# Performance work log

Hardware: AMD Instinct MI355X
Metric: run time of the kernel (lower is better)

The kernel has to match this reference:

```python
import jax, jax.numpy as jnp
import numpy as np

V, D, H, L, E, DH, K, PMAX = 50257, 128, 4, 4, 8, 512, 2, 256
B, T = 8, 256


def setup_inputs() -> dict:
    key = jax.random.key(0)
    ks = jax.random.split(key, 10)
    s = 0.02
    def n(k, shape):
        return jax.random.normal(k, shape, jnp.float32) * s
    return dict(
        idx=jax.random.randint(ks[0], (B, T), 0, V),
        tok_emb=n(ks[1], (V, D)),
        pos_emb=n(ks[2], (PMAX, D)),
        ln1_g=jnp.ones((L, D), jnp.float32), ln1_b=jnp.zeros((L, D), jnp.float32),
        in_w=n(ks[3], (L, 3 * D, D)), in_b=jnp.zeros((L, 3 * D), jnp.float32),
        out_w=n(ks[4], (L, D, D)), out_b=jnp.zeros((L, D), jnp.float32),
        ln2_g=jnp.ones((L, D), jnp.float32), ln2_b=jnp.zeros((L, D), jnp.float32),
        gate_w=n(ks[5], (L, E, D)),
        w1=n(ks[6], (L, E, DH, D)),
        w2=n(ks[7], (L, E, D, DH)),
        lnf_g=jnp.ones((D,), jnp.float32), lnf_b=jnp.zeros((D,), jnp.float32),
        lm_w=n(ks[8], (V, D)),
    )


def _ln(x, g, b):
    mu = x.mean(-1, keepdims=True)
    var = jnp.var(x, -1, keepdims=True)
    return (x - mu) / jnp.sqrt(var + 1e-5) * g + b


def _moe(x, gw, w1, w2):
    # x: [N, D]; top-2 sparse MoE, computed densely per expert then combined.
    logits = x @ gw.T                              # [N, E]
    probs = jax.nn.softmax(logits, -1)
    topw, topi = jax.lax.top_k(probs, K)           # [N, K]
    topw = topw / topw.sum(-1, keepdims=True)
    we = (topw[..., None] * jax.nn.one_hot(topi, E, dtype=x.dtype)).sum(1)  # [N, E]
    h = jax.nn.silu(jnp.einsum('nd,ehd->neh', x, w1))   # [N, E, DH]
    y = jnp.einsum('neh,edh->ned', h, w2)               # [N, E, D]
    return jnp.einsum('ned,ne->nd', y, we)


def reference(idx, tok_emb, pos_emb, ln1_g, ln1_b, in_w, in_b, out_w, out_b,
              ln2_g, ln2_b, gate_w, w1, w2, lnf_g, lnf_b, lm_w):
    b, t = idx.shape
    x = tok_emb[idx] + pos_emb[:t]                 # [B, T, D]
    dh = D // H
    scale = 1.0 / np.sqrt(dh)
    for l in range(L):
        xl = _ln(x, ln1_g[l], ln1_b[l])
        qkv = xl @ in_w[l].T + in_b[l]
        q, k, v = jnp.split(qkv, 3, -1)
        q = q.reshape(b, t, H, dh)
        k = k.reshape(b, t, H, dh)
        v = v.reshape(b, t, H, dh)
        att = jax.nn.softmax(jnp.einsum('bqhd,bkhd->bhqk', q, k) * scale, -1)
        o = jnp.einsum('bhqk,bkhd->bqhd', att, v).reshape(b, t, D)
        x = x + o @ out_w[l].T + out_b[l]
        x2 = _ln(x, ln2_g[l], ln2_b[l]).reshape(b * t, D)
        x = x + _moe(x2, gate_w[l], w1[l], w2[l]).reshape(b, t, D)
    return _ln(x, lnf_g, lnf_b) @ lm_w.T           # [B, T, V]
```

## Files before the change

kernel.cpp:

```cpp
#include <hip/hip_runtime.h>
#include <math.h>

#define NTOK 2048
#define DD   128
#define NHEAD 4
#define DHEAD 32
#define NLAYER 4
#define NEXP 8
#define DHID 512
#define NVOCAB 50257
#define VPAD  50304
#define SEQ   256
#define NBATCH 8

typedef __attribute__((ext_vector_type(8))) short short8v;
typedef __attribute__((ext_vector_type(4))) float f32x4;

__device__ __forceinline__ unsigned short nm_bf16r(float f) {
  unsigned u = __float_as_uint(f);
  u += 0x7fffu + ((u >> 16) & 1u);
  return (unsigned short)(u >> 16);
}

__device__ __forceinline__ float nm_silu(float a) {
  return a / (1.f + __expf(-a));
}

template<int N4>
__device__ __forceinline__ float nm_dotv(const float* __restrict__ a,
                                         const float* __restrict__ w) {
  const float4* a4 = (const float4*)a;
  const float4* w4 = (const float4*)w;
  float sx = 0.f, sy = 0.f, sz = 0.f, sw = 0.f;
#pragma unroll 16
  for (int k = 0; k < N4; ++k) {
    float4 av = a4[k], wv = w4[k];
    sx = fmaf(av.x, wv.x, sx);
    sy = fmaf(av.y, wv.y, sy);
    sz = fmaf(av.z, wv.z, sz);
    sw = fmaf(av.w, wv.w, sw);
  }
  return (sx + sy) + (sz + sw);
}

__global__ void nm_embed(const int* __restrict__ idx, const float* __restrict__ tok,
                         const float* __restrict__ pos, float* __restrict__ x) {
  int n = blockIdx.x, d = threadIdx.x;
  x[n * DD + d] = tok[(size_t)idx[n] * DD + d] + pos[(n % SEQ) * DD + d];
}

__global__ void nm_ln(const float* __restrict__ in, const float* __restrict__ g,
                      const float* __restrict__ b, float* __restrict__ out) {
  int n = blockIdx.x, lane = threadIdx.x;
  float v0 = in[n * DD + lane], v1 = in[n * DD + lane + 64];
  float s = v0 + v1;
#pragma unroll
  for (int o = 32; o > 0; o >>= 1) s += __shfl_xor(s, o, 64);
  float mu = s * (1.f / 128.f);
  float d0 = v0 - mu, d1 = v1 - mu;
  float q = d0 * d0 + d1 * d1;
#pragma unroll
  for (int o = 32; o > 0; o >>= 1) q += __shfl_xor(q, o, 64);
  float rstd = rsqrtf(q * (1.f / 128.f) + 1e-5f);
  out[n * DD + lane]      = d0 * rstd * g[lane]      + b[lane];
  out[n * DD + lane + 64] = d1 * rstd * g[lane + 64] + b[lane + 64];
}

__global__ void nm_combine_ln(const float* __restrict__ yb, const int* __restrict__ posm,
                              const float* __restrict__ topw, float* __restrict__ x,
                              const float* __restrict__ g, const float* __restrict__ b,
                              float* __restrict__ xl) {
  int n = blockIdx.x, lane = threadIdx.x;
  float w0 = topw[2 * n], w1 = topw[2 * n + 1];
  int p0 = posm[2 * n], p1 = posm[2 * n + 1];
  float v0 = x[n * DD + lane]      + w0 * yb[(size_t)p0 * DD + lane]
                                   + w1 * yb[(size_t)p1 * DD + lane];
  float v1 = x[n * DD + lane + 64] + w0 * yb[(size_t)p0 * DD + lane + 64]
                                   + w1 * yb[(size_t)p1 * DD + lane + 64];
  x[n * DD + lane]      = v0;
  x[n * DD + lane + 64] = v1;
  float s = v0 + v1;
#pragma unroll
  for (int o = 32; o > 0; o >>= 1) s += __shfl_xor(s, o, 64);
  float mu = s * (1.f / 128.f);
  float d0 = v0 - mu, d1 = v1 - mu;
  float q = d0 * d0 + d1 * d1;
#pragma unroll
  for (int o = 32; o > 0; o >>= 1) q += __shfl_xor(q, o, 64);
  float rstd = rsqrtf(q * (1.f / 128.f) + 1e-5f);
  xl[n * DD + lane]      = d0 * rstd * g[lane]      + b[lane];
  xl[n * DD + lane + 64] = d1 * rstd * g[lane + 64] + b[lane + 64];
}

template<int F>
__global__ __launch_bounds__(256) void nm_gemm(
    const float* __restrict__ A, const float* __restrict__ B,
    float* __restrict__ C, const float* __restrict__ bias,
    int M, int N, int K,
    const int* __restrict__ list, const int* __restrict__ cnt,
    const int* __restrict__ off) {
  constexpr bool GA = F & 1, SI = F & 2, BI = F & 4, RE = F & 8, GR = F & 16;
  __shared__ __align__(16) float As[64][68];
  __shared__ __align__(16) float Bs[64][68];
  int tid = threadIdx.x;
  int n0 = blockIdx.x * 64, m0 = blockIdx.y * 64;
  int Mloc = M, o = 0;
  const float* Bb = B;
  if constexpr (GR) {
    int e = blockIdx.z;
    Mloc = cnt[e];
    if (m0 >= Mloc) return;
    o = off[e];
    Bb = B + (size_t)e * (size_t)N * K;
  }
  int tm = tid & 15, tn = tid >> 4;
  float acc[4][4] = {};
  for (int kc = 0; kc < K; kc += 64) {
#pragma unroll
    for (int i = 0; i < 4; ++i) {
      int f = tid + 256 * i;
      int r = f >> 4, c4 = f & 15;
      int mi = m0 + r;
      if (mi >= Mloc) mi = m0;
      const float* ar;
      if constexpr (GA) ar = A + (size_t)(list[o + mi] >> 1) * K;
      else              ar = A + (size_t)(o + mi) * K;
      float4 v = *(const float4*)(ar + kc + c4 * 4);
      int k = c4 * 4;
      As[k][r] = v.x; As[k + 1][r] = v.y; As[k + 2][r] = v.z; As[k + 3][r] = v.w;
    }
#pragma unroll
    for (int i = 0; i < 4; ++i) {
      int f = tid + 256 * i;
      int r = f >> 4, c4 = f & 15;
      const float* br = Bb + (size_t)(n0 + r) * K + kc + c4 * 4;
      float4 v = *(const float4*)br;
      int k = c4 * 4;
      Bs[k][r] = v.x; Bs[k + 1][r] = v.y; Bs[k + 2][r] = v.z; Bs[k + 3][r] = v.w;
    }
    __syncthreads();
#pragma unroll 16
    for (int k = 0; k < 64; ++k) {
      float4 a = *(const float4*)&As[k][tm * 4];
      float4 b = *(const float4*)&Bs[k][tn * 4];
      acc[0][0] = fmaf(a.x, b.x, acc[0][0]); acc[0][1] = fmaf(a.x, b.y, acc[0][1]);
      acc[0][2] = fmaf(a.x, b.z, acc[0][2]); acc[0][3] = fmaf(a.x, b.w, acc[0][3]);
      acc[1][0] = fmaf(a.y, b.x, acc[1][0]); acc[1][1] = fmaf(a.y, b.y, acc[1][1]);
      acc[1][2] = fmaf(a.y, b.z, acc[1][2]); acc[1][3] = fmaf(a.y, b.w, acc[1][3]);
      acc[2][0] = fmaf(a.z, b.x, acc[2][0]); acc[2][1] = fmaf(a.z, b.y, acc[2][1]);
      acc[2][2] = fmaf(a.z, b.z, acc[2][2]); acc[2][3] = fmaf(a.z, b.w, acc[2][3]);
      acc[3][0] = fmaf(a.w, b.x, acc[3][0]); acc[3][1] = fmaf(a.w, b.y, acc[3][1]);
      acc[3][2] = fmaf(a.w, b.z, acc[3][2]); acc[3][3] = fmaf(a.w, b.w, acc[3][3]);
    }
    __syncthreads();
  }
  float4 bv = {0.f, 0.f, 0.f, 0.f};
  if constexpr (BI) bv = *(const float4*)(bias + n0 + tn * 4);
#pragma unroll
  for (int i = 0; i < 4; ++i) {
    int mi = m0 + tm * 4 + i;
    if (GR && mi >= Mloc) continue;
    float* cr = C + (size_t)(o + mi) * N + n0 + tn * 4;
    float r0 = acc[i][0], r1 = acc[i][1], r2 = acc[i][2], r3 = acc[i][3];
    if constexpr (BI) { r0 += bv.x; r1 += bv.y; r2 += bv.z; r3 += bv.w; }
    if constexpr (SI) { r0 = nm_silu(r0); r1 = nm_silu(r1); r2 = nm_silu(r2); r3 = nm_silu(r3); }
    if constexpr (RE) { r0 += cr[0]; r1 += cr[1]; r2 += cr[2]; r3 += cr[3]; }
    float4 st = {r0, r1, r2, r3};
    *(float4*)cr = st;
  }
}

__global__ __launch_bounds__(256) void nm_attn2(const float* __restrict__ qkv,
                                                float* __restrict__ o) {
  __shared__ __align__(16) float Ks[SEQ][DHEAD];
  __shared__ __align__(16) float Vs[SEQ][DHEAD];
  __shared__ float mbuf[32][9], sbuf[32][9];
  __shared__ __align__(16) float accbuf[32][36];
  int bh = blockIdx.x;
  int b = bh >> 2, h = bh & 3;
  int qt = blockIdx.y;
  int tid = threadIdx.x;
  const float* base = qkv + (size_t)b * SEQ * 384;
  for (int f = tid; f < SEQ * 8; f += 256) {
    int t = f >> 3, c4 = f & 7;
    float4 kv = *(const float4*)(base + (size_t)t * 384 + 128 + h * DHEAD + c4 * 4);
    float4 vv = *(const float4*)(base + (size_t)t * 384 + 256 + h * DHEAD + c4 * 4);
    *(float4*)&Ks[t][c4 * 4] = kv;
    *(float4*)&Vs[t][c4 * 4] = vv;
  }
  __syncthreads();
  int q = tid & 31, slot = tid >> 5;
  int tq = qt * 32 + q;
  float qv[DHEAD];
  const float4* q4 = (const float4*)(base + (size_t)tq * 384 + h * DHEAD);
#pragma unroll
  for (int k = 0; k < 8; ++k) {
    float4 v = q4[k];
    qv[4*k] = v.x; qv[4*k+1] = v.y; qv[4*k+2] = v.z; qv[4*k+3] = v.w;
  }
  float m = -1e30f, s = 0.f, acc[DHEAD];
#pragma unroll
  for (int d = 0; d < DHEAD; ++d) acc[d] = 0.f;
  const float scale = 0.17677669529663687f;
  int j0 = slot * 32;
  for (int jj = 0; jj < 32; ++jj) {
    int j = j0 + jj;
    const float4* kr = (const float4*)Ks[j];
    float sc = 0.f;
#pragma unroll
    for (int k = 0; k < 8; ++k) {
      float4 v = kr[k];
      sc += qv[4*k]*v.x + qv[4*k+1]*v.y + qv[4*k+2]*v.z + qv[4*k+3]*v.w;
    }
    sc *= scale;
    float mn = fmaxf(m, sc);
    float f = __expf(m - mn), p = __expf(sc - mn);
    s = s * f + p;
    const float4* vr = (const float4*)Vs[j];
#pragma unroll
    for (int k = 0; k < 8; ++k) {
      float4 v = vr[k];
      acc[4*k]   = acc[4*k]  * f + p * v.x;
      acc[4*k+1] = acc[4*k+1]* f + p * v.y;
      acc[4*k+2] = acc[4*k+2]* f + p * v.z;
      acc[4*k+3] = acc[4*k+3]* f + p * v.w;
    }
    m = mn;
  }
  mbuf[q][slot] = m;
  sbuf[q][slot] = s;
  __syncthreads();
  float M = mbuf[q][0];
#pragma unroll
  for (int t = 1; t < 8; ++t) M = fmaxf(M, mbuf[q][t]);
  float S = 0.f;
#pragma unroll
  for (int t = 0; t < 8; ++t) S += sbuf[q][t] * __expf(mbuf[q][t] - M);
  float w = __expf(m - M);
#pragma unroll
  for (int d = 0; d < DHEAD; ++d) acc[d] *= w;
#pragma unroll
  for (int p = 0; p < 8; ++p) {
    if (slot == p) {
      if (p == 0) {
#pragma unroll
        for (int d = 0; d < DHEAD; ++d) accbuf[q][d] = acc[d];
      } else {
#pragma unroll
        for (int d = 0; d < DHEAD; ++d) accbuf[q][d] += acc[d];
      }
    }
    __syncthreads();
  }
  if (slot == 0) sbuf[q][8] = 1.f / S;
  __syncthreads();
  int q2 = tid >> 3, c4 = tid & 7;
  float inv = sbuf[q2][8];
  float4 v = *(const float4*)&accbuf[q2][c4 * 4];
  v.x *= inv; v.y *= inv; v.z *= inv; v.w *= inv;
  *(float4*)(o + (size_t)(b * SEQ + qt * 32 + q2) * DD + h * DHEAD + c4 * 4) = v;
}

__global__ void nm_gate(const float* __restrict__ x2, const float* __restrict__ gw,
                        int* __restrict__ topi, float* __restrict__ topw,
                        int* __restrict__ cnt) {
  int tid = threadIdx.x;
  int e = tid & 7;
  int n = blockIdx.x * 32 + (tid >> 3);
  const float4* xr = (const float4*)(x2 + (size_t)n * DD);
  const float4* wr = (const float4*)(gw + (size_t)e * DD);
  float sx = 0.f, sy = 0.f, sz = 0.f, sw = 0.f;
#pragma unroll
  for (int k = 0; k < 32; ++k) {
    float4 a = xr[k], w = wr[k];
    sx = fmaf(a.x, w.x, sx); sy = fmaf(a.y, w.y, sy);
    sz = fmaf(a.z, w.z, sz); sw = fmaf(a.w, w.w, sw);
  }
  float s = (sx + sy) + (sz + sw);
  int base = (tid & 63) & ~7;
  float g[NEXP];
#pragma unroll
  for (int i = 0; i < NEXP; ++i) g[i] = __shfl(s, base + i, 64);
  if (e == 0) {
    int i0 = 0;
#pragma unroll
    for (int i = 1; i < NEXP; ++i) if (g[i] > g[i0]) i0 = i;
    int i1 = (i0 == 0) ? 1 : 0;
#pragma unroll
    for (int i = 0; i < NEXP; ++i) { if (i != i0 && g[i] > g[i1]) i1 = i; }
    float p1 = __expf(g[i1] - g[i0]);
    float inv = 1.f / (1.f + p1);
    topi[2 * n] = i0; topi[2 * n + 1] = i1;
    topw[2 * n] = inv; topw[2 * n + 1] = p1 * inv;
    atomicAdd(cnt + i0, 1);
    atomicAdd(cnt + i1, 1);
  }
}

__global__ void nm_route(const int* __restrict__ topi, const int* __restrict__ cnt,
                         int* __restrict__ off, int* __restrict__ list,
                         int* __restrict__ posm) {
  __shared__ int lcur[NEXP];
  int tid = threadIdx.x;
  if (tid < NEXP) {
    int o = 0;
    for (int e = 0; e < tid; ++e) o += cnt[e];
    lcur[tid] = o;
    off[tid] = o;
  }
  __syncthreads();
  for (int t = tid; t < 2 * NTOK; t += 1024) {
    int e = topi[t];
    int p = atomicAdd(&lcur[e], 1);
    list[p] = t;
    posm[t] = p;
  }
}

__global__ void nm_zero(int* __restrict__ p, int n) {
  int i = blockIdx.x * 64 + threadIdx.x;
  if (i < n) p[i] = 0;
}

__global__ void nm_moe(const float* __restrict__ x2, const float* __restrict__ gw,
                       const float* __restrict__ w1, const float* __restrict__ w2,
                       float* __restrict__ x) {
  __shared__ __align__(16) float xs[DD];
  __shared__ __align__(16) float hs[DHID];
  __shared__ float gl[NEXP];
  __shared__ int   ei[2];
  __shared__ float ew[2];
  int n = blockIdx.x, tid = threadIdx.x;
  if (tid < DD) xs[tid] = x2[n * DD + tid];
  __syncthreads();
  if (tid < NEXP) gl[tid] = nm_dotv<32>(xs, gw + (size_t)tid * DD);
  __syncthreads();
  if (tid == 0) {
    int i0 = 0;
#pragma unroll
    for (int e = 1; e < NEXP; ++e) if (gl[e] > gl[i0]) i0 = e;
    int i1 = (i0 == 0) ? 1 : 0;
    for (int e = 0; e < NEXP; ++e) { if (e == i0) continue; if (gl[e] > gl[i1]) i1 = e; }
    float p1 = __expf(gl[i1] - gl[i0]);
    float inv = 1.f / (1.f + p1);
    ei[0] = i0; ei[1] = i1; ew[0] = inv; ew[1] = p1 * inv;
  }
  __syncthreads();
  float yacc = 0.f;
  for (int t2 = 0; t2 < 2; ++t2) {
    int e = ei[t2];
    float wt = ew[t2];
    const float* w1e = w1 + (size_t)e * DHID * DD;
#pragma unroll
    for (int jj = 0; jj < 2; ++jj) {
      int j = tid + jj * 256;
      float a = nm_dotv<32>(xs, w1e + (size_t)j * DD);
      hs[j] = nm_silu(a);
    }
    __syncthreads();
    if (tid < DD) yacc += wt * nm_dotv<128>(hs, w2 + ((size_t)e * DD + tid) * DHID);
    __syncthreads();
  }
  if (tid < DD) x[n * DD + tid] += yacc;
}

__global__ void nm_cvt_x(const float* __restrict__ in, unsigned short* __restrict__ ob) {
  int i = blockIdx.x * 256 + threadIdx.x;
  ob[i] = nm_bf16r(in[i]);
}
__global__ void nm_cvt_w(const float* __restrict__ in, unsigned short* __restrict__ ob) {
  size_t i = (size_t)blockIdx.x * 256 + threadIdx.x;
  const size_t n = (size_t)NVOCAB * DD;
  ob[i] = (i < n) ? nm_bf16r(in[i]) : (unsigned short)0;
}

__device__ __forceinline__ short8v nm_load8(const unsigned short* p) {
  return *(const short8v*)p;
}
__device__ __forceinline__ short8v nm_cvt8(const float* p) {
  const float4* p4 = (const float4*)p;
  float4 a = p4[0], b = p4[1];
  short8v r;
  r[0] = (short)nm_bf16r(a.x); r[1] = (short)nm_bf16r(a.y);
  r[2] = (short)nm_bf16r(a.z); r[3] = (short)nm_bf16r(a.w);
  r[4] = (short)nm_bf16r(b.x); r[5] = (short)nm_bf16r(b.y);
  r[6] = (short)nm_bf16r(b.z); r[7] = (short)nm_bf16r(b.w);
  return r;
}

template<bool PRE>
__global__ __launch_bounds__(256) void nm_lmhead(
    const float* __restrict__ xf, const unsigned short* __restrict__ xfb,
    const float* __restrict__ lmw, const unsigned short* __restrict__ lmwb,
    float* __restrict__ out) {
  int wave = threadIdx.x >> 6, lane = threadIdx.x & 63;
  int wr = wave >> 1, wc = wave & 1;
  int row0 = blockIdx.y * 128 + wr * 64;
  int col0 = blockIdx.x * 128 + wc * 64;
  int lr = lane & 15, lk = (lane >> 4) * 8;

  f32x4 acc[4][4] = {};
#pragma unroll
  for (int ks = 0; ks < 4; ++ks) {
    int kb = ks * 32 + lk;
    short8v a[4], b[4];
#pragma unroll
    for (int i = 0; i < 4; ++i) {
      int r = row0 + i * 16 + lr;
      if constexpr (PRE) a[i] = nm_load8(xfb + (size_t)r * DD + kb);
      else               a[i] = nm_cvt8(xf + (size_t)r * DD + kb);
    }
#pragma unroll
    for (int j = 0; j < 4; ++j) {
      int c = col0 + j * 16 + lr;
      if constexpr (PRE) {
        b[j] = nm_load8(lmwb + (size_t)c * DD + kb);
      } else {
        if (c < NVOCAB) b[j] = nm_cvt8(lmw + (size_t)c * DD + kb);
        else {
          short8v z;
#pragma unroll
          for (int e = 0; e < 8; ++e) z[e] = 0;
          b[j] = z;
        }
      }
    }
#pragma unroll
    for (int i = 0; i < 4; ++i)
#pragma unroll
      for (int j = 0; j < 4; ++j)
        acc[i][j] = __builtin_amdgcn_mfma_f32_16x16x32_bf16(a[i], b[j], acc[i][j], 0, 0, 0);
  }
  int cr = (lane >> 4) * 4;
#pragma unroll
  for (int j = 0; j < 4; ++j) {
    int c = col0 + j * 16 + (lane & 15);
    if (c < NVOCAB) {
#pragma unroll
      for (int i = 0; i < 4; ++i)
#pragma unroll
        for (int r = 0; r < 4; ++r)
          out[(size_t)(row0 + i * 16 + cr + r) * NVOCAB + c] = acc[i][j][r];
    }
  }
}

extern "C" void kernel_launch(void* const* d_in, const int* in_sizes, int n_in,
                              void* d_out, int out_size, void* d_ws, size_t ws_size,
                              hipStream_t stream) {
  const int*   idx   = (const int*)  d_in[0];
  const float* tok   = (const float*)d_in[1];
  const float* pos   = (const float*)d_in[2];
  const float* ln1g  = (const float*)d_in[3];
  const float* ln1b  = (const float*)d_in[4];
  const float* inw   = (const float*)d_in[5];
  const float* inb   = (const float*)d_in[6];
  const float* outw  = (const float*)d_in[7];
  const float* outb  = (const float*)d_in[8];
  const float* ln2g  = (const float*)d_in[9];
  const float* ln2b  = (const float*)d_in[10];
  const float* gatew = (const float*)d_in[11];
  const float* w1    = (const float*)d_in[12];
  const float* w2    = (const float*)d_in[13];
  const float* lnfg  = (const float*)d_in[14];
  const float* lnfb  = (const float*)d_in[15];
  const float* lmw   = (const float*)d_in[16];
  float* out = (float*)d_out;

  float* ws   = (float*)d_ws;
  float* x    = ws;
  float* xl   = x    + NTOK * DD;
  float* qkv  = xl   + NTOK * DD;
  float* ao   = qkv  + NTOK * 384;
  float* topw = ao   + NTOK * DD;
  float* H    = topw + 2 * NTOK;
  float* yb   = H    + 2 * NTOK * DHID;
  int*   topi = (int*)(yb + 2 * NTOK * DD);
  int*   list = topi + 2 * NTOK;
  int*   posm = list + 2 * NTOK;
  int*   cnt  = posm + 2 * NTOK;
  int*   offs = cnt  + NLAYER * NEXP;
  unsigned short* xfb  = (unsigned short*)(offs + NLAYER * NEXP);
  unsigned short* lmwb = xfb + NTOK * DD;

  const size_t moe_bytes = (size_t)((char*)xfb - (char*)d_ws);
  const size_t pre_bytes = moe_bytes + ((size_t)NTOK * DD + (size_t)VPAD * DD) * 2;
  const bool moe_ok = (ws_size >= moe_bytes);
  const bool pre = (ws_size >= pre_bytes);

  nm_embed<<<NTOK, DD, 0, stream>>>(idx, tok, pos, x);
  if (moe_ok) nm_zero<<<(NLAYER * NEXP + 63) / 64, 64, 0, stream>>>(cnt, NLAYER * NEXP);
  nm_ln<<<NTOK, 64, 0, stream>>>(x, ln1g, ln1b, xl);

  for (int l = 0; l < NLAYER; ++l) {
    nm_gemm<4><<<dim3(384 / 64, NTOK / 64), 256, 0, stream>>>(
        xl, inw + (size_t)l * 384 * DD, qkv, inb + (size_t)l * 384,
        NTOK, 384, DD, nullptr, nullptr, nullptr);
    nm_attn2<<<dim3(NBATCH * NHEAD, SEQ / 32), 256, 0, stream>>>(qkv, ao);
    nm_gemm<12><<<dim3(DD / 64, NTOK / 64), 256, 0, stream>>>(
        ao, outw + (size_t)l * DD * DD, x, outb + (size_t)l * DD,
        NTOK, DD, DD, nullptr, nullptr, nullptr);
    nm_ln<<<NTOK, 64, 0, stream>>>(x, ln2g + l * DD, ln2b + l * DD, xl);

    const float* gN = (l < NLAYER - 1) ? ln1g + (l + 1) * DD : lnfg;
    const float* bN = (l < NLAYER - 1) ? ln1b + (l + 1) * DD : lnfb;
    if (moe_ok) {
      int* cnt_l = cnt + l * NEXP;
      int* off_l = offs + l * NEXP;
      const float* w1l = w1 + (size_t)l * NEXP * DHID * DD;
      const float* w2l = w2 + (size_t)l * NEXP * DD * DHID;
      nm_gate<<<NTOK / 32, 256, 0, stream>>>(xl, gatew + (size_t)l * NEXP * DD,
                                             topi, topw, cnt_l);
      nm_route<<<1, 1024, 0, stream>>>(topi, cnt_l, off_l, list, posm);
      nm_gemm<19><<<dim3(DHID / 64, 2 * NTOK / 64, NEXP), 256, 0, stream>>>(
          xl, w1l, H, nullptr, 0, DHID, DD, list, cnt_l, off_l);
      nm_gemm<16><<<dim3(DD / 64, 2 * NTOK / 64, NEXP), 256, 0, stream>>>(
          H, w2l, yb, nullptr, 0, DD, DHID, nullptr, cnt_l, off_l);
      nm_combine_ln<<<NTOK, 64, 0, stream>>>(yb, posm, topw, x, gN, bN, xl);
    } else {
      nm_moe<<<NTOK, 256, 0, stream>>>(xl, gatew + (size_t)l * NEXP * DD,
                                       w1 + (size_t)l * NEXP * DHID * DD,
                                       w2 + (size_t)l * NEXP * DD * DHID, x);
      nm_ln<<<NTOK, 64, 0, stream>>>(x, gN, bN, xl);
    }
  }

  if (pre) {
    nm_cvt_x<<<NTOK * DD / 256, 256, 0, stream>>>(xl, xfb);
    nm_cvt_w<<<VPAD * DD / 256, 256, 0, stream>>>(lmw, lmwb);
    nm_lmhead<true><<<dim3(VPAD / 128, NTOK / 128), 256, 0, stream>>>(
        xl, xfb, lmw, lmwb, out);
  } else {
    nm_lmhead<false><<<dim3(VPAD / 128, NTOK / 128), 256, 0, stream>>>(
        xl, nullptr, lmw, nullptr, out);
  }
}
```

Before: 915.3 us.

## Fuse embed+LN, out-proj+LN+gate, bf16 cast into combine, LDS-staged LM head

Embedding and the first LayerNorm now run in one kernel. The out-projection GEMM is fused with the residual add, LN2 and the MoE gate top-2 into a single kernel per layer. The final bf16 activation cast moves into the last combine_ln, and the weight cast is issued early. The LM head stages both bf16 tiles in swizzled LDS before the MFMA loop. Together these remove several launches and intermediate global round-trips. The costs are fewer blocks for the out-proj GEMM and a single-pass variance formula that is slightly less numerically robust.

```diff
diff --git a/kernel.cpp b/kernel.cpp
--- a/kernel.cpp
+++ b/kernel.cpp
@@ -43,10 +43,27 @@
   return (sx + sy) + (sz + sw);
 }
 
-__global__ void nm_embed(const int* __restrict__ idx, const float* __restrict__ tok,
-                         const float* __restrict__ pos, float* __restrict__ x) {
-  int n = blockIdx.x, d = threadIdx.x;
-  x[n * DD + d] = tok[(size_t)idx[n] * DD + d] + pos[(n % SEQ) * DD + d];
+__global__ void nm_embed_ln(const int* __restrict__ idx, const float* __restrict__ tok,
+                            const float* __restrict__ pos, const float* __restrict__ g,
+                            const float* __restrict__ b, float* __restrict__ x,
+                            float* __restrict__ xl) {
+  int n = blockIdx.x, lane = threadIdx.x;
+  int t = idx[n];
+  float v0 = tok[(size_t)t * DD + lane]      + pos[(n % SEQ) * DD + lane];
+  float v1 = tok[(size_t)t * DD + lane + 64] + pos[(n % SEQ) * DD + lane + 64];
+  x[n * DD + lane]      = v0;
+  x[n * DD + lane + 64] = v1;
+  float s = v0 + v1;
+#pragma unroll
+  for (int o = 32; o > 0; o >>= 1) s += __shfl_xor(s, o, 64);
+  float mu = s * (1.f / 128.f);
+  float d0 = v0 - mu, d1 = v1 - mu;
+  float q = d0 * d0 + d1 * d1;
+#pragma unroll
+  for (int o = 32; o > 0; o >>= 1) q += __shfl_xor(q, o, 64);
+  float rstd = rsqrtf(q * (1.f / 128.f) + 1e-5f);
+  xl[n * DD + lane]      = d0 * rstd * g[lane]      + b[lane];
+  xl[n * DD + lane + 64] = d1 * rstd * g[lane + 64] + b[lane + 64];
 }
 
 __global__ void nm_ln(const float* __restrict__ in, const float* __restrict__ g,
@@ -69,7 +86,7 @@
 __global__ void nm_combine_ln(const float* __restrict__ yb, const int* __restrict__ posm,
                               const float* __restrict__ topw, float* __restrict__ x,
                               const float* __restrict__ g, const float* __restrict__ b,
-                              float* __restrict__ xl) {
+                              float* __restrict__ xl, unsigned short* __restrict__ xb) {
   int n = blockIdx.x, lane = threadIdx.x;
   float w0 = topw[2 * n], w1 = topw[2 * n + 1];
   int p0 = posm[2 * n], p1 = posm[2 * n + 1];
@@ -88,8 +105,14 @@
 #pragma unroll
   for (int o = 32; o > 0; o >>= 1) q += __shfl_xor(q, o, 64);
   float rstd = rsqrtf(q * (1.f / 128.f) + 1e-5f);
-  xl[n * DD + lane]      = d0 * rstd * g[lane]      + b[lane];
-  xl[n * DD + lane + 64] = d1 * rstd * g[lane + 64] + b[lane + 64];
+  float o0 = d0 * rstd * g[lane]      + b[lane];
+  float o1 = d1 * rstd * g[lane + 64] + b[lane + 64];
+  xl[n * DD + lane]      = o0;
+  xl[n * DD + lane + 64] = o1;
+  if (xb) {
+    xb[n * DD + lane]      = nm_bf16r(o0);
+    xb[n * DD + lane + 64] = nm_bf16r(o1);
+  }
 }
 
 template<int F>
@@ -170,6 +193,123 @@
   }
 }
 
+__global__ __launch_bounds__(256) void nm_oplng(
+    const float* __restrict__ ao, const float* __restrict__ w,
+    const float* __restrict__ bias, float* __restrict__ x,
+    const float* __restrict__ g, const float* __restrict__ b,
+    float* __restrict__ xl, const float* __restrict__ gw,
+    int* __restrict__ topi, float* __restrict__ topw, int* __restrict__ cnt) {
+  __shared__ __align__(16) float As[64][36];
+  __shared__ __align__(16) float Bs[64][132];
+  __shared__ float Ls[32][9];
+  int tid = threadIdx.x;
+  int m0 = blockIdx.x * 32;
+  int tm = tid >> 5, tn = tid & 31;
+  float acc[4][4] = {};
+  for (int kc = 0; kc < DD; kc += 64) {
+#pragma unroll
+    for (int i = 0; i < 2; ++i) {
+      int ch = tid + 256 * i, r = ch >> 4, c4 = ch & 15;
+      float4 v = *(const float4*)(ao + (size_t)(m0 + r) * DD + kc + c4 * 4);
+      int k = c4 * 4;
+      As[k][r] = v.x; As[k + 1][r] = v.y; As[k + 2][r] = v.z; As[k + 3][r] = v.w;
+    }
+#pragma unroll
+    for (int i = 0; i < 8; ++i) {
+      int ch = tid + 256 * i, r = ch >> 4, c4 = ch & 15;
+      float4 v = *(const float4*)(w + (size_t)r * DD + kc + c4 * 4);
+      int k = c4 * 4;
+      Bs[k][r] = v.x; Bs[k + 1][r] = v.y; Bs[k + 2][r] = v.z; Bs[k + 3][r] = v.w;
+    }
+    __syncthreads();
+#pragma unroll 8
+    for (int k = 0; k < 64; ++k) {
+      float4 a = *(const float4*)&As[k][tm * 4];
+      float4 bb = *(const float4*)&Bs[k][tn * 4];
+      acc[0][0] = fmaf(a.x, bb.x, acc[0][0]); acc[0][1] = fmaf(a.x, bb.y, acc[0][1]);
+      acc[0][2] = fmaf(a.x, bb.z, acc[0][2]); acc[0][3] = fmaf(a.x, bb.w, acc[0][3]);
+      acc[1][0] = fmaf(a.y, bb.x, acc[1][0]); acc[1][1] = fmaf(a.y, bb.y, acc[1][1]);
+      acc[1][2] = fmaf(a.y, bb.z, acc[1][2]); acc[1][3] = fmaf(a.y, bb.w, acc[1][3]);
+      acc[2][0] = fmaf(a.z, bb.x, acc[2][0]); acc[2][1] = fmaf(a.z, bb.y, acc[2][1]);
+      acc[2][2] = fmaf(a.z, bb.z, acc[2][2]); acc[2][3] = fmaf(a.z, bb.w, acc[2][3]);
+      acc[3][0] = fmaf(a.w, bb.x, acc[3][0]); acc[3][1] = fmaf(a.w, bb.y, acc[3][1]);
+      acc[3][2] = fmaf(a.w, bb.z, acc[3][2]); acc[3][3] = fmaf(a.w, bb.w, acc[3][3]);
+    }
+    __syncthreads();
+  }
+  float4 bv = *(const float4*)(bias + tn * 4);
+  float rr[4][4], s1[4], s2[4];
+#pragma unroll
+  for (int i = 0; i < 4; ++i) {
+    int rw = m0 + tm * 4 + i;
+    float4 xv = *(const float4*)(x + (size_t)rw * DD + tn * 4);
+    float r0 = acc[i][0] + bv.x + xv.x;
+    float r1 = acc[i][1] + bv.y + xv.y;
+    float r2 = acc[i][2] + bv.z + xv.z;
+    float r3 = acc[i][3] + bv.w + xv.w;
+    rr[i][0] = r0; rr[i][1] = r1; rr[i][2] = r2; rr[i][3] = r3;
+    float4 st = {r0, r1, r2, r3};
+    *(float4*)(x + (size_t)rw * DD + tn * 4) = st;
+    s1[i] = r0 + r1 + r2 + r3;
+    s2[i] = r0 * r0 + r1 * r1 + r2 * r2 + r3 * r3;
+  }
+#pragma unroll
+  for (int o = 16; o >= 1; o >>= 1) {
+#pragma unroll
+    for (int i = 0; i < 4; ++i) {
+      s1[i] += __shfl_xor(s1[i], o, 64);
+      s2[i] += __shfl_xor(s2[i], o, 64);
+    }
+  }
+  float4 gv  = *(const float4*)(g + tn * 4);
+  float4 bbv = *(const float4*)(b + tn * 4);
+#pragma unroll
+  for (int i = 0; i < 4; ++i) {
+    int rw = m0 + tm * 4 + i;
+    float mu = s1[i] * (1.f / 128.f);
+    float var = s2[i] * (1.f / 128.f) - mu * mu;
+    float rstd = rsqrtf(var + 1e-5f);
+    float y0 = (rr[i][0] - mu) * rstd * gv.x + bbv.x;
+    float y1 = (rr[i][1] - mu) * rstd * gv.y + bbv.y;
+    float y2 = (rr[i][2] - mu) * rstd * gv.z + bbv.z;
+    float y3 = (rr[i][3] - mu) * rstd * gv.w + bbv.w;
+    float4 yv = {y0, y1, y2, y3};
+    *(float4*)(xl + (size_t)rw * DD + tn * 4) = yv;
+    *(float4*)&Bs[tm * 4 + i][tn * 4] = yv;
+  }
+  __syncthreads();
+  int grow = tid >> 3, ge = tid & 7;
+  const float4* xr = (const float4*)&Bs[grow][0];
+  const float4* wr = (const float4*)(gw + (size_t)ge * DD);
+  float sx = 0.f, sy = 0.f, sz = 0.f, sw = 0.f;
+#pragma unroll
+  for (int k2 = 0; k2 < 32; ++k2) {
+    float4 a = xr[k2], w4 = wr[k2];
+    sx = fmaf(a.x, w4.x, sx); sy = fmaf(a.y, w4.y, sy);
+    sz = fmaf(a.z, w4.z, sz); sw = fmaf(a.w, w4.w, sw);
+  }
+  Ls[grow][ge] = (sx + sy) + (sz + sw);
+  __syncthreads();
+  if (ge == 0) {
+    float gl[NEXP];
+#pragma unroll
+    for (int e = 0; e < NEXP; ++e) gl[e] = Ls[grow][e];
+    int i0 = 0;
+#pragma unroll
+    for (int e = 1; e < NEXP; ++e) if (gl[e] > gl[i0]) i0 = e;
+    int i1 = (i0 == 0) ? 1 : 0;
+#pragma unroll
+    for (int e = 0; e < NEXP; ++e) { if (e != i0 && gl[e] > gl[i1]) i1 = e; }
+    float p1 = __expf(gl[i1] - gl[i0]);
+    float inv = 1.f / (1.f + p1);
+    int n = m0 + grow;
+    topi[2 * n] = i0; topi[2 * n + 1] = i1;
+    topw[2 * n] = inv; topw[2 * n + 1] = p1 * inv;
+    atomicAdd(cnt + i0, 1);
+    atomicAdd(cnt + i1, 1);
+  }
+}
+
 __global__ __launch_bounds__(256) void nm_attn2(const float* __restrict__ qkv,
                                                 float* __restrict__ o) {
   __shared__ __align__(16) float Ks[SEQ][DHEAD];
@@ -261,42 +401,6 @@
   *(float4*)(o + (size_t)(b * SEQ + qt * 32 + q2) * DD + h * DHEAD + c4 * 4) = v;
 }
 
-__global__ void nm_gate(const float* __restrict__ x2, const float* __restrict__ gw,
-                        int* __restrict__ topi, float* __restrict__ topw,
-                        int* __restrict__ cnt) {
-  int tid = threadIdx.x;
-  int e = tid & 7;
-  int n = blockIdx.x * 32 + (tid >> 3);
-  const float4* xr = (const float4*)(x2 + (size_t)n * DD);
-  const float4* wr = (const float4*)(gw + (size_t)e * DD);
-  float sx = 0.f, sy = 0.f, sz = 0.f, sw = 0.f;
-#pragma unroll
-  for (int k = 0; k < 32; ++k) {
-    float4 a = xr[k], w = wr[k];
-    sx = fmaf(a.x, w.x, sx); sy = fmaf(a.y, w.y, sy);
-    sz = fmaf(a.z, w.z, sz); sw = fmaf(a.w, w.w, sw);
-  }
-  float s = (sx + sy) + (sz + sw);
-  int base = (tid & 63) & ~7;
-  float g[NEXP];
-#pragma unroll
-  for (int i = 0; i < NEXP; ++i) g[i] = __shfl(s, base + i, 64);
-  if (e == 0) {
-    int i0 = 0;
-#pragma unroll
-    for (int i = 1; i < NEXP; ++i) if (g[i] > g[i0]) i0 = i;
-    int i1 = (i0 == 0) ? 1 : 0;
-#pragma unroll
-    for (int i = 0; i < NEXP; ++i) { if (i != i0 && g[i] > g[i1]) i1 = i; }
-    float p1 = __expf(g[i1] - g[i0]);
-    float inv = 1.f / (1.f + p1);
-    topi[2 * n] = i0; topi[2 * n + 1] = i1;
-    topw[2 * n] = inv; topw[2 * n + 1] = p1 * inv;
-    atomicAdd(cnt + i0, 1);
-    atomicAdd(cnt + i1, 1);
-  }
-}
-
 __global__ void nm_route(const int* __restrict__ topi, const int* __restrict__ cnt,
                          int* __restrict__ off, int* __restrict__ list,
                          int* __restrict__ posm) {
@@ -364,19 +468,12 @@
   if (tid < DD) x[n * DD + tid] += yacc;
 }
 
-__global__ void nm_cvt_x(const float* __restrict__ in, unsigned short* __restrict__ ob) {
-  int i = blockIdx.x * 256 + threadIdx.x;
-  ob[i] = nm_bf16r(in[i]);
-}
 __global__ void nm_cvt_w(const float* __restrict__ in, unsigned short* __restrict__ ob) {
   size_t i = (size_t)blockIdx.x * 256 + threadIdx.x;
   const size_t n = (size_t)NVOCAB * DD;
   ob[i] = (i < n) ? nm_bf16r(in[i]) : (unsigned short)0;
 }
 
-__device__ __forceinline__ short8v nm_load8(const unsigned short* p) {
-  return *(const short8v*)p;
-}
 __device__ __forceinline__ short8v nm_cvt8(const float* p) {
   const float4* p4 = (const float4*)p;
   float4 a = p4[0], b = p4[1];
@@ -388,41 +485,84 @@
   return r;
 }
 
-template<bool PRE>
-__global__ __launch_bounds__(256) void nm_lmhead(
-    const float* __restrict__ xf, const unsigned short* __restrict__ xfb,
-    const float* __restrict__ lmw, const unsigned short* __restrict__ lmwb,
+__global__ __launch_bounds__(256) void nm_lmhead2(
+    const unsigned short* __restrict__ xfb, const unsigned short* __restrict__ lmwb,
+    float* __restrict__ out) {
+  __shared__ unsigned short Ab[128 * 128];
+  __shared__ unsigned short Bb[128 * 128];
+  int tid = threadIdx.x;
+  int row0 = blockIdx.y * 128, col0 = blockIdx.x * 128;
+#pragma unroll
+  for (int i = 0; i < 8; ++i) {
+    int ch = tid + i * 256;
+    int r = ch >> 4, s = ch & 15;
+    int sg = s ^ (r & 7);
+    *(short8v*)&Ab[r * 128 + s * 8] =
+        *(const short8v*)(xfb + (size_t)(row0 + r) * DD + sg * 8);
+    *(short8v*)&Bb[r * 128 + s * 8] =
+        *(const short8v*)(lmwb + (size_t)(col0 + r) * DD + sg * 8);
+  }
+  __syncthreads();
+  int wave = tid >> 6, lane = tid & 63;
+  int wr = wave >> 1, wc = wave & 1;
+  int lr = lane & 15, hk = lane >> 4;
+  f32x4 acc[4][4] = {};
+#pragma unroll
+  for (int ks = 0; ks < 4; ++ks) {
+    int sg = ks * 4 + hk;
+    int sx = (sg ^ (lr & 7)) * 8;
+    short8v a[4], b[4];
+#pragma unroll
+    for (int i = 0; i < 4; ++i)
+      a[i] = *(const short8v*)&Ab[(wr * 64 + i * 16 + lr) * 128 + sx];
+#pragma unroll
+    for (int j = 0; j < 4; ++j)
+      b[j] = *(const short8v*)&Bb[(wc * 64 + j * 16 + lr) * 128 + sx];
+#pragma unroll
+    for (int i = 0; i < 4; ++i)
+#pragma unroll
+      for (int j = 0; j < 4; ++j)
+        acc[i][j] = __builtin_amdgcn_mfma_f32_16x16x32_bf16(a[i], b[j], acc[i][j], 0, 0, 0);
+  }
+  int cr = (lane >> 4) * 4;
+#pragma unroll
+  for (int j = 0; j < 4; ++j) {
+    int c = col0 + wc * 64 + j * 16 + (lane & 15);
+    if (c < NVOCAB) {
+#pragma unroll
+      for (int i = 0; i < 4; ++i)
+#pragma unroll
+        for (int r = 0; r < 4; ++r)
+          out[(size_t)(row0 + wr * 64 + i * 16 + cr + r) * NVOCAB + c] = acc[i][j][r];
+    }
+  }
+}
+
+__global__ __launch_bounds__(256) void nm_lmhead_f32(
+    const float* __restrict__ xf, const float* __restrict__ lmw,
     float* __restrict__ out) {
   int wave = threadIdx.x >> 6, lane = threadIdx.x & 63;
   int wr = wave >> 1, wc = wave & 1;
   int row0 = blockIdx.y * 128 + wr * 64;
   int col0 = blockIdx.x * 128 + wc * 64;
   int lr = lane & 15, lk = (lane >> 4) * 8;
-
   f32x4 acc[4][4] = {};
 #pragma unroll
   for (int ks = 0; ks < 4; ++ks) {
     int kb = ks * 32 + lk;
     short8v a[4], b[4];
 #pragma unroll
-    for (int i = 0; i < 4; ++i) {
-      int r = row0 + i * 16 + lr;
-      if constexpr (PRE) a[i] = nm_load8(xfb + (size_t)r * DD + kb);
-      else               a[i] = nm_cvt8(xf + (size_t)r * DD + kb);
-    }
+    for (int i = 0; i < 4; ++i)
+      a[i] = nm_cvt8(xf + (size_t)(row0 + i * 16 + lr) * DD + kb);
 #pragma unroll
     for (int j = 0; j < 4; ++j) {
       int c = col0 + j * 16 + lr;
-      if constexpr (PRE) {
-        b[j] = nm_load8(lmwb + (size_t)c * DD + kb);
-      } else {
-        if (c < NVOCAB) b[j] = nm_cvt8(lmw + (size_t)c * DD + kb);
-        else {
-          short8v z;
-#pragma unroll
-          for (int e = 0; e < 8; ++e) z[e] = 0;
-          b[j] = z;
-        }
+      if (c < NVOCAB) b[j] = nm_cvt8(lmw + (size_t)c * DD + kb);
+      else {
+        short8v z;
+#pragma unroll
+        for (int e = 0; e < 8; ++e) z[e] = 0;
+        b[j] = z;
       }
     }
 #pragma unroll
@@ -473,14 +613,14 @@
   float* qkv  = xl   + NTOK * DD;
   float* ao   = qkv  + NTOK * 384;
   float* topw = ao   + NTOK * DD;
-  float* H    = topw + 2 * NTOK;
-  float* yb   = H    + 2 * NTOK * DHID;
-  int*   topi = (int*)(yb + 2 * NTOK * DD);
+  int*   topi = (int*)(topw + 2 * NTOK);
   int*   list = topi + 2 * NTOK;
   int*   posm = list + 2 * NTOK;
   int*   cnt  = posm + 2 * NTOK;
   int*   offs = cnt  + NLAYER * NEXP;
-  unsigned short* xfb  = (unsigned short*)(offs + NLAYER * NEXP);
+  float* H    = (float*)(offs + NLAYER * NEXP);
+  float* yb   = H    + 2 * NTOK * DHID;
+  unsigned short* xfb  = (unsigned short*)(yb + 2 * NTOK * DD);
   unsigned short* lmwb = xfb + NTOK * DD;
 
   const size_t moe_bytes = (size_t)((char*)xfb - (char*)d_ws);
@@ -488,19 +628,19 @@
   const bool moe_ok = (ws_size >= moe_bytes);
   const bool pre = (ws_size >= pre_bytes);
 
-  nm_embed<<<NTOK, DD, 0, stream>>>(idx, tok, pos, x);
+  nm_embed_ln<<<NTOK, 64, 0, stream>>>(idx, tok, pos, ln1g, ln1b, x, xl);
   if (moe_ok) nm_zero<<<(NLAYER * NEXP + 63) / 64, 64, 0, stream>>>(cnt, NLAYER * NEXP);
-  nm_ln<<<NTOK, 64, 0, stream>>>(x, ln1g, ln1b, xl);
+  if (pre) nm_cvt_w<<<VPAD * DD / 256, 256, 0, stream>>>(lmw, lmwb);
 
   for (int l = 0; l < NLAYER; ++l) {
     nm_gemm<4><<<dim3(384 / 64, NTOK / 64), 256, 0, stream>>>(
         xl, inw + (size_t)l * 384 * DD, qkv, inb + (size_t)l * 384,
         NTOK, 384, DD, nullptr, nullptr, nullptr);
     nm_attn2<<<dim3(NBATCH * NHEAD, SEQ / 32), 256, 0, stream>>>(qkv, ao);
-    nm_gemm<12><<<dim3(DD / 64, NTOK / 64), 256, 0, stream>>>(
-        ao, outw + (size_t)l * DD * DD, x, outb + (size_t)l * DD,
-        NTOK, DD, DD, nullptr, nullptr, nullptr);
-    nm_ln<<<NTOK, 64, 0, stream>>>(x, ln2g + l * DD, ln2b + l * DD, xl);
+    nm_oplng<<<NTOK / 32, 256, 0, stream>>>(
+        ao, outw + (size_t)l * DD * DD, outb + (size_t)l * DD, x,
+        ln2g + l * DD, ln2b + l * DD, xl, gatew + (size_t)l * NEXP * DD,
+        topi, topw, cnt + l * NEXP);
 
     const float* gN = (l < NLAYER - 1) ? ln1g + (l + 1) * DD : lnfg;
     const float* bN = (l < NLAYER - 1) ? ln1b + (l + 1) * DD : lnfb;
@@ -509,14 +649,14 @@
       int* off_l = offs + l * NEXP;
       const float* w1l = w1 + (size_t)l * NEXP * DHID * DD;
       const float* w2l = w2 + (size_t)l * NEXP * DD * DHID;
-      nm_gate<<<NTOK / 32, 256, 0, stream>>>(xl, gatew + (size_t)l * NEXP * DD,
-                                             topi, topw, cnt_l);
       nm_route<<<1, 1024, 0, stream>>>(topi, cnt_l, off_l, list, posm);
       nm_gemm<19><<<dim3(DHID / 64, 2 * NTOK / 64, NEXP), 256, 0, stream>>>(
           xl, w1l, H, nullptr, 0, DHID, DD, list, cnt_l, off_l);
       nm_gemm<16><<<dim3(DD / 64, 2 * NTOK / 64, NEXP), 256, 0, stream>>>(
           H, w2l, yb, nullptr, 0, DD, DHID, nullptr, cnt_l, off_l);
-      nm_combine_ln<<<NTOK, 64, 0, stream>>>(yb, posm, topw, x, gN, bN, xl);
+      nm_combine_ln<<<NTOK, 64, 0, stream>>>(
+          yb, posm, topw, x, gN, bN, xl,
+          (l == NLAYER - 1 && pre) ? xfb : (unsigned short*)nullptr);
     } else {
       nm_moe<<<NTOK, 256, 0, stream>>>(xl, gatew + (size_t)l * NEXP * DD,
                                        w1 + (size_t)l * NEXP * DHID * DD,
@@ -526,12 +666,8 @@
   }
 
   if (pre) {
-    nm_cvt_x<<<NTOK * DD / 256, 256, 0, stream>>>(xl, xfb);
-    nm_cvt_w<<<VPAD * DD / 256, 256, 0, stream>>>(lmw, lmwb);
-    nm_lmhead<true><<<dim3(VPAD / 128, NTOK / 128), 256, 0, stream>>>(
-        xl, xfb, lmw, lmwb, out);
+    nm_lmhead2<<<dim3(VPAD / 128, NTOK / 128), 256, 0, stream>>>(xfb, lmwb, out);
   } else {
-    nm_lmhead<false><<<dim3(VPAD / 128, NTOK / 128), 256, 0, stream>>>(
-        xl, nullptr, lmw, nullptr, out);
-  }
-}
+    nm_lmhead_f32<<<dim3(VPAD / 128, NTOK / 128), 256, 0, stream>>>(xl, lmw, out);
+  }
+}
```

Measured after the change: 848.9 us. 7.3% less time.
